# Kernel optimization log

Measured on AMD Instinct MI355X. Metric: run time of the kernel, lower is better.

Reference implementation:

```python
import jax, jax.numpy as jnp
import numpy as np

N, E = 50000, 800000
IN_C, OUT_C = 128, 64
HID = 2 * OUT_C


def _sage_conv(x, src, dst, n_nodes, W_l, b_l, W_r):
    # PyG SAGEConv (mean aggr, root_weight=True, normalize=False):
    # out = lin_l(mean_{j in N(i)} x_j) + lin_r(x_i)
    msgs = x[src]                                            # [E, d]
    agg = jax.ops.segment_sum(msgs, dst, num_segments=n_nodes)
    cnt = jax.ops.segment_sum(jnp.ones((src.shape[0],), x.dtype), dst,
                              num_segments=n_nodes)
    agg = agg / jnp.maximum(cnt, 1.0)[:, None]               # mean (0 if no nbrs)
    return agg @ W_l + b_l + x @ W_r


def setup_inputs() -> dict:
    key = jax.random.key(0)
    ks = jax.random.split(key, 8)
    x = jax.random.normal(ks[0], (N, IN_C), dtype=jnp.float32)
    edge_index = jax.random.randint(ks[1], (2, E), 0, N, dtype=jnp.int64)
    s1 = 1.0 / np.sqrt(IN_C)
    s2 = 1.0 / np.sqrt(HID)
    W1_l = jax.random.uniform(ks[2], (IN_C, HID), jnp.float32, -s1, s1)
    W1_r = jax.random.uniform(ks[3], (IN_C, HID), jnp.float32, -s1, s1)
    b1 = jax.random.uniform(ks[4], (HID,), jnp.float32, -s1, s1)
    W2_l = jax.random.uniform(ks[5], (HID, OUT_C), jnp.float32, -s2, s2)
    W2_r = jax.random.uniform(ks[6], (HID, OUT_C), jnp.float32, -s2, s2)
    b2 = jax.random.uniform(ks[7], (OUT_C,), jnp.float32, -s2, s2)
    return {"x": x, "edge_index": edge_index,
            "W1_l": W1_l, "b1": b1, "W1_r": W1_r,
            "W2_l": W2_l, "b2": b2, "W2_r": W2_r}


def reference(x, edge_index, W1_l, b1, W1_r, W2_l, b2, W2_r):
    src, dst = edge_index[0], edge_index[1]
    n_nodes = x.shape[0]
    h = _sage_conv(x, src, dst, n_nodes, W1_l, b1, W1_r)
    h = jax.nn.relu(h)
    return _sage_conv(h, src, dst, n_nodes, W2_l, b2, W2_r)
```

## Files before the change

### kernel.cpp

```cpp
#include <hip/hip_runtime.h>


#define K_IN 128
#define CAP  80

typedef float f32x4 __attribute__((ext_vector_type(4)));
typedef short bf16x8 __attribute__((ext_vector_type(8)));

static __device__ __forceinline__ unsigned short f2bf(float f) {
    unsigned int u = __float_as_uint(f);
    u = (u + 0x7FFFu + ((u >> 16) & 1u)) >> 16;
    return (unsigned short)u;
}
static __device__ __forceinline__ float bf2f(unsigned short s) {
    return __uint_as_float(((unsigned int)s) << 16);
}

__global__ __launch_bounds__(256) void k_build(const int* __restrict__ src,
                                               const int* __restrict__ dst, int E,
                                               int* __restrict__ cnt,
                                               int* __restrict__ ebuf,
                                               const float* __restrict__ W1l,
                                               const float* __restrict__ W1r,
                                               const float* __restrict__ W2l,
                                               const float* __restrict__ W2r,
                                               short* __restrict__ Wt1,
                                               short* __restrict__ Wt2, int nbe) {
    int b = blockIdx.x;
    if (b < nbe) {
        int stride = nbe * 256;
        for (int i = b * 256 + threadIdx.x; i < E; i += stride) {
            int s = src[i];
            int d = dst[i];
            int p = atomicAdd(&cnt[d], 1);
            if (p < CAP) ebuf[d * CAP + p] = s;
        }
    } else {
        int t = (b - nbe) * 256 + threadIdx.x;
        int tot1 = 256 * 128, tot2 = 128 * 128;
        if (t < tot1) {
            int j = t >> 7, k = t & 127;
            float v = (j < 128) ? W1l[k * 128 + j] : W1r[k * 128 + (j - 128)];
            Wt1[t] = (short)f2bf(v);
        } else if (t < tot1 + tot2) {
            int u = t - tot1;
            int j = u >> 7, k = u & 127;
            float v = (j < 64) ? W2l[k * 64 + j] : W2r[k * 64 + (j - 64)];
            Wt2[u] = (short)f2bf(v);
        }
    }
}


template <bool ABF16>
__device__ __forceinline__ void load_tile(const void* __restrict__ Av, int row0,
                                          int nrows, int t, float4* rf, int4* ri) {
    if (ABF16) {
        const short* A = (const short*)Av;
#pragma unroll
        for (int it = 0; it < 4; ++it) {
            int c = it * 256 + t;
            int r = c >> 4, c8 = c & 15;
            int4 v = make_int4(0, 0, 0, 0);
            if (row0 + r < nrows)
                v = *reinterpret_cast<const int4*>(A + (size_t)(row0 + r) * 128 + c8 * 8);
            ri[it] = v;
        }
    } else {
        const float* A = (const float*)Av;
#pragma unroll
        for (int it = 0; it < 8; ++it) {
            int c = it * 256 + t;
            int r = c >> 5, c4 = c & 31;
            float4 v = make_float4(0.f, 0.f, 0.f, 0.f);
            if (row0 + r < nrows)
                v = *reinterpret_cast<const float4*>(A + (size_t)(row0 + r) * 128 + c4 * 4);
            rf[it] = v;
        }
    }
}

template <bool ABF16>
__device__ __forceinline__ void lds_tile(short (*buf)[136], int t,
                                         const float4* rf, const int4* ri) {
    if (ABF16) {
#pragma unroll
        for (int it = 0; it < 4; ++it) {
            int c = it * 256 + t;
            int r = c >> 4, c8 = c & 15;
            *reinterpret_cast<int4*>(&buf[r][c8 * 8]) = ri[it];
        }
    } else {
#pragma unroll
        for (int it = 0; it < 8; ++it) {
            int c = it * 256 + t;
            int r = c >> 5, c4 = c & 31;
            float4 v = rf[it];
            ushort4 o;
            o.x = f2bf(v.x); o.y = f2bf(v.y); o.z = f2bf(v.z); o.w = f2bf(v.w);
            *reinterpret_cast<ushort4*>(&buf[r][c4 * 4]) = o;
        }
    }
}

template <int NC, bool ABF16>
__global__ __launch_bounds__(256, 2) void k_gemm(const void* __restrict__ Av,
                                                 const short* __restrict__ Wt,
                                                 short* __restrict__ outL,
                                                 float* __restrict__ outR, int nrows) {
    constexpr int WC = NC / 4;
    constexpr int BR = WC / 16;
    constexpr int HC = NC / 2;
    __shared__ short sA[2][64][136];

    int t = threadIdx.x;
    int wid = t >> 6, lane = t & 63, qk = lane >> 4, ln = lane & 15;
    int ntiles = (nrows + 63) >> 6;
    int nPB = gridDim.x;

    int tile = (int)blockIdx.x;
    if (tile >= ntiles) return;

    const short* Wb = Wt + (size_t)(wid * WC + ln) * 128 + qk * 8;
    bf16x8 breg[4][BR];
#pragma unroll
    for (int kk = 0; kk < 4; ++kk)
#pragma unroll
        for (int br = 0; br < BR; ++br)
            breg[kk][br] = *reinterpret_cast<const bf16x8*>(Wb + br * 16 * 128 + kk * 32);

    float4 rf[8];
    int4   ri[4];

    load_tile<ABF16>(Av, tile * 64, nrows, t, rf, ri);
    lds_tile<ABF16>(sA[0], t, rf, ri);
    __syncthreads();

    int cur = 0;
    while (true) {
        int next = tile + nPB;
        bool hasNext = (next < ntiles);
        if (hasNext) load_tile<ABF16>(Av, next * 64, nrows, t, rf, ri);

        int row0 = tile * 64;
        f32x4 acc[4][BR];
#pragma unroll
        for (int ar = 0; ar < 4; ++ar)
#pragma unroll
            for (int br = 0; br < BR; ++br) acc[ar][br] = (f32x4)(0.0f);

#pragma unroll
        for (int kk = 0; kk < 4; ++kk) {
            bf16x8 a[4];
#pragma unroll
            for (int ar = 0; ar < 4; ++ar)
                a[ar] = *reinterpret_cast<const bf16x8*>(&sA[cur][ar * 16 + ln][kk * 32 + qk * 8]);
#pragma unroll
            for (int br = 0; br < BR; ++br)
#pragma unroll
                for (int ar = 0; ar < 4; ++ar)
                    acc[ar][br] = __builtin_amdgcn_mfma_f32_16x16x32_bf16(
                        a[ar], breg[kk][br], acc[ar][br], 0, 0, 0);
        }

#pragma unroll
        for (int ar = 0; ar < 4; ++ar)
#pragma unroll
            for (int br = 0; br < BR; ++br) {
                int gcol = wid * WC + br * 16 + ln;
#pragma unroll
                for (int r = 0; r < 4; ++r) {
                    int grow = row0 + ar * 16 + qk * 4 + r;
                    if (grow < nrows) {
                        float v = acc[ar][br][r];
                        if (gcol < HC)
                            outL[(size_t)grow * HC + gcol] = (short)f2bf(v);
                        else
                            outR[(size_t)grow * HC + (gcol - HC)] = v;
                    }
                }
            }

        if (!hasNext) break;
        lds_tile<ABF16>(sA[cur ^ 1], t, rf, ri);
        __syncthreads();
        cur ^= 1;
        tile = next;
    }
}

__global__ __launch_bounds__(256) void agg_relu_128(const short* __restrict__ y1l,
                                                    const float* __restrict__ y1r,
                                                    const int* __restrict__ cnt,
                                                    const int* __restrict__ ebuf,
                                                    const float* __restrict__ bias,
                                                    short* __restrict__ h, int n) {
    int i = blockIdx.x * 4 + (threadIdx.x >> 6);
    if (i >= n) return;
    int lane = threadIdx.x & 63;
    int g = lane >> 4, l = lane & 15;
    int deg = cnt[i]; if (deg > CAP) deg = CAP;
    const int* eb = ebuf + (size_t)i * CAP;
    float a[8];
#pragma unroll
    for (int j = 0; j < 8; ++j) a[j] = 0.f;

    for (int e = g; e < deg; e += 4) {
        int s = eb[e];
        bf16x8 v = *reinterpret_cast<const bf16x8*>(y1l + (size_t)s * 128 + l * 8);
#pragma unroll
        for (int j = 0; j < 8; ++j) a[j] += bf2f((unsigned short)v[j]);
    }
#pragma unroll
    for (int j = 0; j < 8; ++j) {
        a[j] += __shfl_xor(a[j], 16);
        a[j] += __shfl_xor(a[j], 32);
    }
    if (g == 0) {
        float inv = 1.0f / fmaxf((float)deg, 1.0f);
        int c0 = l * 8;
        const float* rr = y1r + (size_t)i * 128 + c0;
        const float* bb = bias + c0;
        unsigned int pk[4];
#pragma unroll
        for (int j2 = 0; j2 < 4; ++j2) {
            float o0 = fmaxf(a[j2 * 2]     * inv + bb[j2 * 2]     + rr[j2 * 2],     0.0f);
            float o1 = fmaxf(a[j2 * 2 + 1] * inv + bb[j2 * 2 + 1] + rr[j2 * 2 + 1], 0.0f);
            pk[j2] = (unsigned int)f2bf(o0) | ((unsigned int)f2bf(o1) << 16);
        }
        *reinterpret_cast<int4*>(h + (size_t)i * 128 + c0) =
            make_int4((int)pk[0], (int)pk[1], (int)pk[2], (int)pk[3]);
    }
}

__global__ __launch_bounds__(256) void agg_64(const short* __restrict__ z2l,
                                              const int* __restrict__ cnt,
                                              const int* __restrict__ ebuf,
                                              const float* __restrict__ bias,
                                              float* __restrict__ out, int n) {
    int i = blockIdx.x * 4 + (threadIdx.x >> 6);
    if (i >= n) return;
    int lane = threadIdx.x & 63;
    int g = lane >> 3, l = lane & 7;
    int deg = cnt[i]; if (deg > CAP) deg = CAP;
    const int* eb = ebuf + (size_t)i * CAP;
    float a[8];
#pragma unroll
    for (int j = 0; j < 8; ++j) a[j] = 0.f;

    for (int e = g; e < deg; e += 8) {
        int s = eb[e];
        bf16x8 v = *reinterpret_cast<const bf16x8*>(z2l + (size_t)s * 64 + l * 8);
#pragma unroll
        for (int j = 0; j < 8; ++j) a[j] += bf2f((unsigned short)v[j]);
    }
#pragma unroll
    for (int j = 0; j < 8; ++j) {
        a[j] += __shfl_xor(a[j], 8);
        a[j] += __shfl_xor(a[j], 16);
        a[j] += __shfl_xor(a[j], 32);
    }
    if (g == 0) {
        float inv = 1.0f / fmaxf((float)deg, 1.0f);
        int c0 = l * 8;
        float* op = out + (size_t)i * 64 + c0;
        const float* bb = bias + c0;
#pragma unroll
        for (int j = 0; j < 8; ++j) op[j] = a[j] * inv + bb[j] + op[j];
    }
}


extern "C" void kernel_launch(void* const* d_in, const int* in_sizes, int n_in,
                              void* d_out, int out_size, void* d_ws, size_t ws_size,
                              hipStream_t stream) {
    const float* x   = (const float*)d_in[0];
    const int*   ei  = (const int*)d_in[1];
    const float* W1l = (const float*)d_in[2];
    const float* b1  = (const float*)d_in[3];
    const float* W1r = (const float*)d_in[4];
    const float* W2l = (const float*)d_in[5];
    const float* b2  = (const float*)d_in[6];
    const float* W2r = (const float*)d_in[7];
    float* out = (float*)d_out;

    int n = in_sizes[0] / K_IN;
    int E = in_sizes[1] / 2;
    const int* src = ei;
    const int* dst = ei + E;

    size_t off = 0;
    char* base = (char*)d_ws;
    auto alloc = [&](size_t bytes) {
        void* q = base + off;
        off += (bytes + 255) & ~(size_t)255;
        return q;
    };
    int*   cnt  = (int*)alloc((size_t)n * 4);
    int*   ebuf = (int*)alloc((size_t)n * CAP * 4);
    short* Wt1  = (short*)alloc(256 * 128 * 2);
    short* Wt2  = (short*)alloc(128 * 128 * 2);
    short* y1l  = (short*)alloc((size_t)n * 128 * 2);
    float* y1r  = (float*)alloc((size_t)n * 128 * 4);
    short* h    = (short*)alloc((size_t)n * 128 * 2);
    short* z2l  = y1l;
    (void)ws_size; (void)n_in; (void)out_size;

    hipMemsetAsync(cnt, 0, (size_t)n * 4, stream);

    int nbe = (E + 255) / 256;
    int npw = (256 * 128 + 128 * 128 + 255) / 256;
    k_build<<<nbe + npw, 256, 0, stream>>>(src, dst, E, cnt, ebuf,
                                           W1l, W1r, W2l, W2r, Wt1, Wt2, nbe);

    k_gemm<256, false><<<512, 256, 0, stream>>>(x, Wt1, y1l, y1r, n);
    agg_relu_128<<<(n + 3) / 4, 256, 0, stream>>>(y1l, y1r, cnt, ebuf, b1, h, n);

    k_gemm<128, true><<<512, 256, 0, stream>>>(h, Wt2, z2l, out, n);
    agg_64<<<(n + 3) / 4, 256, 0, stream>>>(z2l, cnt, ebuf, b2, out, n);
}
```

Measured before the change: 220.3 us.

## Partition adjacency build by destination slice and shrink bucket capacity to 64

The edge bucketing kernel now has 8 block groups. Each group scans all edges with int4 loads but only inserts edges whose destination falls in its node slice, which keeps atomics and ebuf writes in a smaller, more cache-local region (likely per-XCD L2 given the block-id modulo 8). Bucket capacity drops from 80 to 64 so indexing can use shifts and the bucket buffer shrinks. The cost is reading dst eight times over, and a risk of dropping neighbors for nodes with in-degree above 64, which is unlikely with mean degree 16.

```diff
diff --git a/kernel.cpp b/kernel.cpp
--- a/kernel.cpp
+++ b/kernel.cpp
@@ -2,7 +2,8 @@
 
 
 #define K_IN 128
-#define CAP  80
+#define CAP  64
+#define LG_CAP 6
 
 typedef float f32x4 __attribute__((ext_vector_type(4)));
 typedef short bf16x8 __attribute__((ext_vector_type(8)));
@@ -18,6 +19,7 @@
 
 __global__ __launch_bounds__(256) void k_build(const int* __restrict__ src,
                                                const int* __restrict__ dst, int E,
+                                               int n,
                                                int* __restrict__ cnt,
                                                int* __restrict__ ebuf,
                                                const float* __restrict__ W1l,
@@ -25,18 +27,42 @@
                                                const float* __restrict__ W2l,
                                                const float* __restrict__ W2r,
                                                short* __restrict__ Wt1,
-                                               short* __restrict__ Wt2, int nbe) {
+                                               short* __restrict__ Wt2, int nbb) {
     int b = blockIdx.x;
-    if (b < nbe) {
-        int stride = nbe * 256;
-        for (int i = b * 256 + threadIdx.x; i < E; i += stride) {
-            int s = src[i];
-            int d = dst[i];
-            int p = atomicAdd(&cnt[d], 1);
-            if (p < CAP) ebuf[d * CAP + p] = s;
+    if (b < nbb) {
+        int g = b & 7;
+        int sliceN = (n + 7) >> 3;
+        int lo = g * sliceN;
+        int hi = lo + sliceN; if (hi > n) hi = n;
+        int tid = (b >> 3) * 256 + threadIdx.x;
+        int nv4 = E >> 2;
+        const int4* s4 = (const int4*)src;
+        const int4* d4 = (const int4*)dst;
+        for (int i = tid; i < nv4; i += 256 * 256) {
+            int4 d = d4[i];
+            bool ix = (d.x >= lo) & (d.x < hi);
+            bool iy = (d.y >= lo) & (d.y < hi);
+            bool iz = (d.z >= lo) & (d.z < hi);
+            bool iw = (d.w >= lo) & (d.w < hi);
+            if (ix | iy | iz | iw) {
+                int4 s = s4[i];
+                if (ix) { int p = atomicAdd(&cnt[d.x], 1); if (p < CAP) ebuf[(d.x << LG_CAP) + p] = s.x; }
+                if (iy) { int p = atomicAdd(&cnt[d.y], 1); if (p < CAP) ebuf[(d.y << LG_CAP) + p] = s.y; }
+                if (iz) { int p = atomicAdd(&cnt[d.z], 1); if (p < CAP) ebuf[(d.z << LG_CAP) + p] = s.z; }
+                if (iw) { int p = atomicAdd(&cnt[d.w], 1); if (p < CAP) ebuf[(d.w << LG_CAP) + p] = s.w; }
+            }
+        }
+        if ((b >> 3) == 0 && threadIdx.x == 0) {
+            for (int i = nv4 << 2; i < E; ++i) {
+                int d = dst[i];
+                if (d >= lo && d < hi) {
+                    int p = atomicAdd(&cnt[d], 1);
+                    if (p < CAP) ebuf[(d << LG_CAP) + p] = src[i];
+                }
+            }
         }
     } else {
-        int t = (b - nbe) * 256 + threadIdx.x;
+        int t = (b - nbb) * 256 + threadIdx.x;
         int tot1 = 256 * 128, tot2 = 128 * 128;
         if (t < tot1) {
             int j = t >> 7, k = t & 127;
@@ -200,7 +226,7 @@
     int lane = threadIdx.x & 63;
     int g = lane >> 4, l = lane & 15;
     int deg = cnt[i]; if (deg > CAP) deg = CAP;
-    const int* eb = ebuf + (size_t)i * CAP;
+    const int* eb = ebuf + ((size_t)i << LG_CAP);
     float a[8];
 #pragma unroll
     for (int j = 0; j < 8; ++j) a[j] = 0.f;
@@ -243,7 +269,7 @@
     int lane = threadIdx.x & 63;
     int g = lane >> 3, l = lane & 7;
     int deg = cnt[i]; if (deg > CAP) deg = CAP;
-    const int* eb = ebuf + (size_t)i * CAP;
+    const int* eb = ebuf + ((size_t)i << LG_CAP);
     float a[8];
 #pragma unroll
     for (int j = 0; j < 8; ++j) a[j] = 0.f;
@@ -308,10 +334,10 @@
 
     hipMemsetAsync(cnt, 0, (size_t)n * 4, stream);
 
-    int nbe = (E + 255) / 256;
+    const int nbb = 2048;
     int npw = (256 * 128 + 128 * 128 + 255) / 256;
-    k_build<<<nbe + npw, 256, 0, stream>>>(src, dst, E, cnt, ebuf,
-                                           W1l, W1r, W2l, W2r, Wt1, Wt2, nbe);
+    k_build<<<nbb + npw, 256, 0, stream>>>(src, dst, E, n, cnt, ebuf,
+                                           W1l, W1r, W2l, W2r, Wt1, Wt2, nbb);
 
     k_gemm<256, false><<<512, 256, 0, stream>>>(x, Wt1, y1l, y1r, n);
     agg_relu_128<<<(n + 3) / 4, 256, 0, stream>>>(y1l, y1r, cnt, ebuf, b1, h, n);
```

Result: faster. 212.2 us (-3.7%).
